# Kernel tuning notes

Measured on AMD Instinct MI355X. Metric: run time of the kernel, lower is better.

## Reference

```python
import jax, jax.numpy as jnp
import numpy as np

H, D = 16, 64  # num_heads, head_dim (hidden = H*D = 1024)
EPS = 1e-6

def elu_plus_one(x):
    return jax.nn.elu(x) + 1.0

def setup_inputs() -> dict:
    key = jax.random.key(0)
    ks = jax.random.split(key, 12)
    hid = H * D
    s = 0.02
    return {
        "hidden_states": jax.random.normal(ks[0], (1, 2048, hid), jnp.float32),
        "w_q": jax.random.normal(ks[1], (hid, hid), jnp.float32) * s,
        "w_k": jax.random.normal(ks[2], (hid, hid), jnp.float32) * s,
        "w_v": jax.random.normal(ks[3], (hid, hid), jnp.float32) * s,
        "w_o": jax.random.normal(ks[4], (hid, hid), jnp.float32) * s,
        "memory_gate": jnp.zeros((H,), jnp.float32),
        "eg_w1": jax.random.normal(ks[5], (hid, hid // 4), jnp.float32) * s,
        "eg_b1": jnp.zeros((hid // 4,), jnp.float32),
        "eg_w2": jax.random.normal(ks[6], (hid // 4, 1), jnp.float32) * s,
        "eg_b2": jnp.zeros((1,), jnp.float32),
        "fine_mem": jax.random.normal(ks[7], (4, H, D, D), jnp.float32) * s,
        "fine_norm": jax.random.uniform(ks[8], (4, H, D), jnp.float32),
    }

def _retrieve(sigma_q, memory, memory_norm):
    # sigma_q: [b,h,s,d], memory: [h,d,e], memory_norm: [h,d]
    a = jnp.einsum('bhsd,hde->bhse', sigma_q, memory)
    relevance = jnp.einsum('bhsd,hd->bhs', sigma_q, memory_norm)
    out = a / jnp.clip(relevance, EPS, None)[..., None]
    return out, relevance

def reference(hidden_states, w_q, w_k, w_v, w_o, memory_gate,
              eg_w1, eg_b1, eg_w2, eg_b2, fine_mem, fine_norm):
    B, S, hid = hidden_states.shape
    def proj(w):
        return (hidden_states @ w).reshape(B, S, H, D).transpose(0, 2, 1, 3)  # [b,h,s,d]
    q, k, v = proj(w_q), proj(w_k), proj(w_v)
    sigma_q = elu_plus_one(q)

    # coarse memory = sum of fine memories
    M_coarse = fine_mem.sum(0)        # [h,d,d]
    z_coarse = fine_norm.sum(0)       # [h,d]
    output_coarse, _ = _retrieve(sigma_q, M_coarse, z_coarse)  # [b,h,s,d]

    # learned expansion gate on coarse representation
    coarse_repr = output_coarse.transpose(0, 2, 1, 3).reshape(B, S, hid)
    logit = jax.nn.relu(coarse_repr @ eg_w1 + eg_b1) @ eg_w2 + eg_b2  # [b,s,1]
    expansion_prob = jax.nn.sigmoid(logit)                            # [b,s,1]

    # fine-grained retrieval: attention-weighted mix over the 4 banks
    outs = jnp.einsum('bhsd,fhde->fbhse', sigma_q, fine_mem)   # [f,b,h,s,d]
    rels = jnp.einsum('bhsd,fhd->fbhs', sigma_q, fine_norm)    # [f,b,h,s]
    outs = outs / jnp.clip(rels, EPS, None)[..., None]
    weights = jax.nn.softmax(rels.mean(-1), axis=0)            # [f,b,h]
    output_fine = (outs * weights[:, :, :, None, None]).sum(0)  # [b,h,s,d]

    ep = expansion_prob.transpose(0, 2, 1)[..., None]          # [b,1,s,1]
    memory_output = ep * output_fine + (1.0 - ep) * output_coarse

    # causal linear attention within current segment
    sigma_k = elu_plus_one(k)
    kv = jnp.einsum('bhsd,bhse->bhsde', sigma_k, v)            # [b,h,s,d,d]
    kv_cumsum = jnp.cumsum(kv, axis=2)
    k_cumsum = jnp.cumsum(sigma_k, axis=2)
    num = jnp.einsum('bhsd,bhsde->bhse', sigma_q, kv_cumsum)
    den = jnp.clip(jnp.einsum('bhsd,bhsd->bhs', sigma_q, k_cumsum), EPS, None)[..., None]
    local_output = num / den

    gate = jax.nn.sigmoid(memory_gate).reshape(1, H, 1, 1)
    output = gate * memory_output + (1.0 - gate) * local_output
    output = output.transpose(0, 2, 1, 3).reshape(B, S, hid)
    return output @ w_o
```

## Files before the change

kernel.cpp:

```cpp
#include <hip/hip_runtime.h>
#include <cmath>

#define EPSF 1e-6f
#define LDK 72


typedef __attribute__((ext_vector_type(8))) short bf16x8;
typedef __attribute__((ext_vector_type(4))) float f32x4;
typedef __attribute__((ext_vector_type(8))) unsigned short u16x8;

__device__ __forceinline__ float wave_allsum(float v) {
#pragma unroll
  for (int off = 32; off > 0; off >>= 1) v += __shfl_xor(v, off, 64);
  return v;
}

__device__ __forceinline__ unsigned short f2bf(float f) {
  unsigned int u = __float_as_uint(f);
  unsigned int r = (u + 0x7fffu + ((u >> 16) & 1u)) >> 16;
  return (unsigned short)r;
}
__device__ __forceinline__ float bf2f(unsigned short u) {
  return __uint_as_float(((unsigned int)u) << 16);
}

__global__ __launch_bounds__(256) void k0_mcT(const float* __restrict__ FM,
    const float* __restrict__ FN, unsigned short* __restrict__ MCT,
    float* __restrict__ ZC)
{
  int h = blockIdx.x, q = blockIdx.y, tid = threadIdx.x;
  __shared__ float tile[16][65];
  for (int i = tid; i < 1024; i += 256) {
    int dpl = i >> 6, e = i & 63;
    int idx = (q * 16 + dpl) * 64 + e;
    float s = FM[(0 * 16 + h) * 4096 + idx] + FM[(1 * 16 + h) * 4096 + idx]
            + FM[(2 * 16 + h) * 4096 + idx] + FM[(3 * 16 + h) * 4096 + idx];
    tile[dpl][e] = s;
  }
  if (q == 0 && tid < 64)
    ZC[h * 64 + tid] = FN[h * 64 + tid] + FN[1024 + h * 64 + tid]
                     + FN[2048 + h * 64 + tid] + FN[3072 + h * 64 + tid];
  __syncthreads();
  for (int i = tid; i < 1024; i += 256) {
    int e = i >> 4, dpl = i & 15;
    MCT[h * 4096 + e * 64 + q * 16 + dpl] = f2bf(tile[dpl][e]);
  }
}

__global__ __launch_bounds__(256) void cast_bf16_k(const float* __restrict__ X,
    unsigned short* __restrict__ Y)
{
  int i = blockIdx.x * 256 + threadIdx.x;
  float4 v = *reinterpret_cast<const float4*>(X + i * 4);
  ushort4 o; o.x = f2bf(v.x); o.y = f2bf(v.y); o.z = f2bf(v.z); o.w = f2bf(v.w);
  *reinterpret_cast<ushort4*>(Y + i * 4) = o;
}

__global__ __launch_bounds__(256) void cast_transpose_k(const float* __restrict__ W,
    unsigned short* __restrict__ WT, int N)
{
  __shared__ float tile[64][65];
  int n0 = blockIdx.x * 64, k0 = blockIdx.y * 64;
  int tid = threadIdx.x;
  for (int i = tid; i < 4096; i += 256) {
    int r = i >> 6, c = i & 63;
    tile[r][c] = W[(k0 + r) * N + n0 + c];
  }
  __syncthreads();
  for (int i = tid; i < 1024; i += 256) {
    int r = i >> 4, c4 = (i & 15) * 4;
    ushort4 o;
    o.x = f2bf(tile[c4 + 0][r]); o.y = f2bf(tile[c4 + 1][r]);
    o.z = f2bf(tile[c4 + 2][r]); o.w = f2bf(tile[c4 + 3][r]);
    *reinterpret_cast<ushort4*>(&WT[(n0 + r) * 1024 + k0 + c4]) = o;
  }
}

__global__ __launch_bounds__(256) void cast_w4(const float* __restrict__ W0,
    const float* __restrict__ W1, const float* __restrict__ W2, const float* __restrict__ W3,
    unsigned short* __restrict__ T0, unsigned short* __restrict__ T1,
    unsigned short* __restrict__ T2, unsigned short* __restrict__ T3)
{
  int z = blockIdx.z;
  const float* W = (z == 0) ? W0 : (z == 1) ? W1 : (z == 2) ? W2 : W3;
  unsigned short* WT = (z == 0) ? T0 : (z == 1) ? T1 : (z == 2) ? T2 : T3;
  __shared__ float tile[64][65];
  int n0 = blockIdx.x * 64, k0 = blockIdx.y * 64;
  int tid = threadIdx.x;
  for (int i = tid; i < 4096; i += 256) {
    int r = i >> 6, c = i & 63;
    tile[r][c] = W[(k0 + r) * 1024 + n0 + c];
  }
  __syncthreads();
  for (int i = tid; i < 1024; i += 256) {
    int r = i >> 4, c4 = (i & 15) * 4;
    ushort4 o;
    o.x = f2bf(tile[c4 + 0][r]); o.y = f2bf(tile[c4 + 1][r]);
    o.z = f2bf(tile[c4 + 2][r]); o.w = f2bf(tile[c4 + 3][r]);
    *reinterpret_cast<ushort4*>(&WT[(n0 + r) * 1024 + k0 + c4]) = o;
  }
}

__global__ __launch_bounds__(256) void fm_cast_t(const float* __restrict__ FM,
    unsigned short* __restrict__ FMT)
{
  __shared__ float tile[64][65];
  int b = blockIdx.x, tid = threadIdx.x;
  const float* src = FM + b * 4096;
  for (int i = tid; i < 4096; i += 256) tile[i >> 6][i & 63] = src[i];
  __syncthreads();
  unsigned short* dst = FMT + b * 4096;
  for (int i = tid; i < 4096; i += 256) {
    int e = i >> 6, dp = i & 63;
    dst[e * 64 + dp] = f2bf(tile[dp][e]);
  }
}

__global__ __launch_bounds__(256) void mm_bf16(const unsigned short* __restrict__ A,
    const unsigned short* __restrict__ BT, float* __restrict__ C, int ldc, int act)
{
  __shared__ unsigned short As[128 * LDK];
  __shared__ unsigned short Bs[128 * LDK];
  int tid = threadIdx.x;
  int m0 = blockIdx.y * 128, n0 = blockIdx.x * 128;
  int wid = tid >> 6, lane = tid & 63;
  int wr = wid >> 1, wc = wid & 1;
  int lr = lane & 15, lg = lane >> 4;

  f32x4 acc[4][4];
#pragma unroll
  for (int m = 0; m < 4; ++m)
#pragma unroll
    for (int n = 0; n < 4; ++n)
#pragma unroll
      for (int r = 0; r < 4; ++r) acc[m][n][r] = 0.f;

  for (int kt = 0; kt < 16; ++kt) {
    int k0 = kt * 64;
#pragma unroll
    for (int p = 0; p < 4; ++p) {
      int c = p * 256 + tid;
      int row = c >> 3, k8 = c & 7;
      u16x8 va = *reinterpret_cast<const u16x8*>(A + (m0 + row) * 1024 + k0 + k8 * 8);
      *reinterpret_cast<u16x8*>(&As[row * LDK + k8 * 8]) = va;
      u16x8 vb = *reinterpret_cast<const u16x8*>(BT + (n0 + row) * 1024 + k0 + k8 * 8);
      *reinterpret_cast<u16x8*>(&Bs[row * LDK + k8 * 8]) = vb;
    }
    __syncthreads();
#pragma unroll
    for (int kk = 0; kk < 2; ++kk) {
      bf16x8 af[4], bfr[4];
#pragma unroll
      for (int m = 0; m < 4; ++m)
        af[m] = *reinterpret_cast<const bf16x8*>(&As[(wr * 64 + m * 16 + lr) * LDK + kk * 32 + lg * 8]);
#pragma unroll
      for (int n = 0; n < 4; ++n)
        bfr[n] = *reinterpret_cast<const bf16x8*>(&Bs[(wc * 64 + n * 16 + lr) * LDK + kk * 32 + lg * 8]);
#pragma unroll
      for (int m = 0; m < 4; ++m)
#pragma unroll
        for (int n = 0; n < 4; ++n)
          acc[m][n] = __builtin_amdgcn_mfma_f32_16x16x32_bf16(af[m], bfr[n], acc[m][n], 0, 0, 0);
    }
    __syncthreads();
  }
#pragma unroll
  for (int m = 0; m < 4; ++m)
#pragma unroll
    for (int n = 0; n < 4; ++n)
#pragma unroll
      for (int r = 0; r < 4; ++r) {
        float v = acc[m][n][r];
        if (act) v = v > 0.f ? v + 1.f : expf(v);
        C[(m0 + wr * 64 + m * 16 + lg * 4 + r) * ldc + n0 + wc * 64 + n * 16 + lr] = v;
      }
}

__global__ __launch_bounds__(256) void mm_gate_bf16(const unsigned short* __restrict__ MOB,
    const unsigned short* __restrict__ LOB, const float* __restrict__ MG,
    const unsigned short* __restrict__ BT, float* __restrict__ C)
{
  __shared__ unsigned short As[128 * LDK];
  __shared__ unsigned short Bs[128 * LDK];
  __shared__ float gs[16];
  int tid = threadIdx.x;
  int m0 = blockIdx.y * 128, n0 = blockIdx.x * 128;
  int wid = tid >> 6, lane = tid & 63;
  int wr = wid >> 1, wc = wid & 1;
  int lr = lane & 15, lg = lane >> 4;
  if (tid < 16) gs[tid] = 1.f / (1.f + expf(-MG[tid]));
  __syncthreads();

  f32x4 acc[4][4];
#pragma unroll
  for (int m = 0; m < 4; ++m)
#pragma unroll
    for (int n = 0; n < 4; ++n)
#pragma unroll
      for (int r = 0; r < 4; ++r) acc[m][n][r] = 0.f;

  for (int kt = 0; kt < 16; ++kt) {
    int k0 = kt * 64;
#pragma unroll
    for (int p = 0; p < 4; ++p) {
      int c = p * 256 + tid;
      int row = c >> 3, k8 = c & 7;
      int col = k0 + k8 * 8;
      float g = gs[col >> 6];
      u16x8 mv = *reinterpret_cast<const u16x8*>(MOB + (m0 + row) * 1024 + col);
      u16x8 lv = *reinterpret_cast<const u16x8*>(LOB + (m0 + row) * 1024 + col);
      u16x8 o;
#pragma unroll
      for (int j = 0; j < 8; ++j)
        o[j] = f2bf(g * bf2f((unsigned short)mv[j]) + (1.f - g) * bf2f((unsigned short)lv[j]));
      *reinterpret_cast<u16x8*>(&As[row * LDK + k8 * 8]) = o;
      u16x8 vb = *reinterpret_cast<const u16x8*>(BT + (n0 + row) * 1024 + k0 + k8 * 8);
      *reinterpret_cast<u16x8*>(&Bs[row * LDK + k8 * 8]) = vb;
    }
    __syncthreads();
#pragma unroll
    for (int kk = 0; kk < 2; ++kk) {
      bf16x8 af[4], bfr[4];
#pragma unroll
      for (int m = 0; m < 4; ++m)
        af[m] = *reinterpret_cast<const bf16x8*>(&As[(wr * 64 + m * 16 + lr) * LDK + kk * 32 + lg * 8]);
#pragma unroll
      for (int n = 0; n < 4; ++n)
        bfr[n] = *reinterpret_cast<const bf16x8*>(&Bs[(wc * 64 + n * 16 + lr) * LDK + kk * 32 + lg * 8]);
#pragma unroll
      for (int m = 0; m < 4; ++m)
#pragma unroll
        for (int n = 0; n < 4; ++n)
          acc[m][n] = __builtin_amdgcn_mfma_f32_16x16x32_bf16(af[m], bfr[n], acc[m][n], 0, 0, 0);
    }
    __syncthreads();
  }
#pragma unroll
  for (int m = 0; m < 4; ++m)
#pragma unroll
    for (int n = 0; n < 4; ++n)
#pragma unroll
      for (int r = 0; r < 4; ++r)
        C[(m0 + wr * 64 + m * 16 + lg * 4 + r) * 1024 + n0 + wc * 64 + n * 16 + lr] = acc[m][n][r];
}

__global__ __launch_bounds__(256) void proj_bf16(const unsigned short* __restrict__ A,
    const unsigned short* __restrict__ WqT, const unsigned short* __restrict__ WkT,
    const unsigned short* __restrict__ WvT,
    unsigned short* __restrict__ Oq, unsigned short* __restrict__ Ok,
    unsigned short* __restrict__ Ov)
{
  int z = blockIdx.z;
  const unsigned short* BT = (z == 0) ? WqT : (z == 1) ? WkT : WvT;
  unsigned short* C = (z == 0) ? Oq : (z == 1) ? Ok : Ov;

  __shared__ unsigned short As[128 * LDK];
  __shared__ unsigned short Bs[128 * LDK];
  int tid = threadIdx.x;
  int m0 = blockIdx.y * 128, n0 = blockIdx.x * 128;
  int wid = tid >> 6, lane = tid & 63;
  int wr = wid >> 1, wc = wid & 1;
  int lr = lane & 15, lg = lane >> 4;
  int act = (z < 2) ? 1 : 0;

  f32x4 acc[4][4];
#pragma unroll
  for (int m = 0; m < 4; ++m)
#pragma unroll
    for (int n = 0; n < 4; ++n)
#pragma unroll
      for (int r = 0; r < 4; ++r) acc[m][n][r] = 0.f;

  for (int kt = 0; kt < 16; ++kt) {
    int k0 = kt * 64;
#pragma unroll
    for (int p = 0; p < 4; ++p) {
      int c = p * 256 + tid;
      int row = c >> 3, k8 = c & 7;
      u16x8 va = *reinterpret_cast<const u16x8*>(A + (m0 + row) * 1024 + k0 + k8 * 8);
      *reinterpret_cast<u16x8*>(&As[row * LDK + k8 * 8]) = va;
      u16x8 vb = *reinterpret_cast<const u16x8*>(BT + (n0 + row) * 1024 + k0 + k8 * 8);
      *reinterpret_cast<u16x8*>(&Bs[row * LDK + k8 * 8]) = vb;
    }
    __syncthreads();
#pragma unroll
    for (int kk = 0; kk < 2; ++kk) {
      bf16x8 af[4], bfr[4];
#pragma unroll
      for (int m = 0; m < 4; ++m)
        af[m] = *reinterpret_cast<const bf16x8*>(&As[(wr * 64 + m * 16 + lr) * LDK + kk * 32 + lg * 8]);
#pragma unroll
      for (int n = 0; n < 4; ++n)
        bfr[n] = *reinterpret_cast<const bf16x8*>(&Bs[(wc * 64 + n * 16 + lr) * LDK + kk * 32 + lg * 8]);
#pragma unroll
      for (int m = 0; m < 4; ++m)
#pragma unroll
        for (int n = 0; n < 4; ++n)
          acc[m][n] = __builtin_amdgcn_mfma_f32_16x16x32_bf16(af[m], bfr[n], acc[m][n], 0, 0, 0);
    }
    __syncthreads();
  }
#pragma unroll
  for (int m = 0; m < 4; ++m)
#pragma unroll
    for (int n = 0; n < 4; ++n)
#pragma unroll
      for (int r = 0; r < 4; ++r) {
        float v = acc[m][n][r];
        if (act) v = v > 0.f ? v + 1.f : expf(v);
        C[(m0 + wr * 64 + m * 16 + lg * 4 + r) * 1024 + n0 + wc * 64 + n * 16 + lr] = f2bf(v);
      }
}

__global__ __launch_bounds__(256) void eg_fin(const float* __restrict__ H1,
    const float* __restrict__ B1, const float* __restrict__ W2,
    const float* __restrict__ B2, float* __restrict__ EP)
{
  int wid = threadIdx.x >> 6, lane = threadIdx.x & 63;
  int s = blockIdx.x * 4 + wid;
  float4 h = *reinterpret_cast<const float4*>(H1 + s * 256 + lane * 4);
  float4 b = *reinterpret_cast<const float4*>(B1 + lane * 4);
  float4 w = *reinterpret_cast<const float4*>(W2 + lane * 4);
  float v = fmaxf(h.x + b.x, 0.f) * w.x + fmaxf(h.y + b.y, 0.f) * w.y
          + fmaxf(h.z + b.z, 0.f) * w.z + fmaxf(h.w + b.w, 0.f) * w.w;
  v = wave_allsum(v);
  if (lane == 0) EP[s] = 1.f / (1.f + expf(-(v + B2[0])));
}

__global__ __launch_bounds__(256) void rels_kernel(const unsigned short* __restrict__ SQB,
    const float* __restrict__ ZC, const float* __restrict__ FN,
    float* __restrict__ RELC, float* __restrict__ RELS, float* __restrict__ PARTS)
{
  int h = blockIdx.x, st = blockIdx.y, tid = threadIdx.x;
  int s0 = st * 64;
  __shared__ float sqT[64][68];
  __shared__ float zf[5][64];
  __shared__ float relb[5][64];
#pragma unroll
  for (int p = 0; p < 2; ++p) {
    int cidx = p * 256 + tid;
    int r = cidx >> 3, d8 = cidx & 7;
    u16x8 v = *reinterpret_cast<const u16x8*>(SQB + (s0 + r) * 1024 + h * 64 + d8 * 8);
#pragma unroll
    for (int j = 0; j < 8; ++j) sqT[d8 * 8 + j][r] = bf2f((unsigned short)v[j]);
  }
  for (int idx = tid; idx < 320; idx += 256) {
    int w = idx >> 6, d = idx & 63;
    zf[w][d] = (w == 0) ? ZC[h * 64 + d] : FN[(w - 1) * 1024 + h * 64 + d];
  }
  __syncthreads();
  {
    int s = tid & 63, wh = tid >> 6;
    float r = 0.f;
    for (int dp = 0; dp < 64; ++dp) r += sqT[dp][s] * zf[wh][dp];
    relb[wh][s] = r;
    if (wh == 0) {
      float r4 = 0.f;
      for (int dp = 0; dp < 64; ++dp) r4 += sqT[dp][s] * zf[4][dp];
      relb[4][s] = r4;
    }
  }
  __syncthreads();
  if (tid < 64) {
    RELC[h * 2048 + s0 + tid] = relb[0][tid];
#pragma unroll
    for (int f = 0; f < 4; ++f)
      RELS[f * 32768 + h * 2048 + s0 + tid] = relb[1 + f][tid];
#pragma unroll
    for (int f = 0; f < 4; ++f) {
      float v = wave_allsum(relb[1 + f][tid]);
      if (tid == 0) PARTS[f * 512 + h * 32 + st] = v;
    }
  }
}

__global__ __launch_bounds__(256) void coarse_mfma(const unsigned short* __restrict__ SQB,
    const unsigned short* __restrict__ MCT, const float* __restrict__ RELC,
    unsigned short* __restrict__ COB)
{
  int h = blockIdx.x, st = blockIdx.y, tid = threadIdx.x;
  int w = tid >> 6, lane = tid & 63, lr = lane & 15, lg = lane >> 4;
  int s0 = st * 128;
  __shared__ unsigned short A_lds[128 * LDK];
  __shared__ unsigned short B_lds[64 * LDK];
#pragma unroll
  for (int p = 0; p < 4; ++p) {
    int c = p * 256 + tid;
    int row = c >> 3, k8 = c & 7;
    *reinterpret_cast<u16x8*>(&A_lds[row * LDK + k8 * 8]) =
        *reinterpret_cast<const u16x8*>(SQB + (s0 + row) * 1024 + h * 64 + k8 * 8);
  }
#pragma unroll
  for (int p = 0; p < 2; ++p) {
    int c = p * 256 + tid;
    int e = c >> 3, k8 = c & 7;
    *reinterpret_cast<u16x8*>(&B_lds[e * LDK + k8 * 8]) =
        *reinterpret_cast<const u16x8*>(MCT + h * 4096 + e * 64 + k8 * 8);
  }
  __syncthreads();

  f32x4 acc[2][4];
#pragma unroll
  for (int m = 0; m < 2; ++m)
#pragma unroll
    for (int n = 0; n < 4; ++n)
#pragma unroll
      for (int r = 0; r < 4; ++r) acc[m][n][r] = 0.f;

#pragma unroll
  for (int kk = 0; kk < 2; ++kk) {
    bf16x8 af[2], bfr[4];
#pragma unroll
    for (int m = 0; m < 2; ++m)
      af[m] = *reinterpret_cast<const bf16x8*>(&A_lds[(w * 32 + m * 16 + lr) * LDK + kk * 32 + lg * 8]);
#pragma unroll
    for (int n = 0; n < 4; ++n)
      bfr[n] = *reinterpret_cast<const bf16x8*>(&B_lds[(n * 16 + lr) * LDK + kk * 32 + lg * 8]);
#pragma unroll
    for (int m = 0; m < 2; ++m)
#pragma unroll
      for (int n = 0; n < 4; ++n)
        acc[m][n] = __builtin_amdgcn_mfma_f32_16x16x32_bf16(af[m], bfr[n], acc[m][n], 0, 0, 0);
  }
#pragma unroll
  for (int m = 0; m < 2; ++m)
#pragma unroll
    for (int r = 0; r < 4; ++r) {
      int s = s0 + w * 32 + m * 16 + lg * 4 + r;
      float rc = fmaxf(RELC[h * 2048 + s], EPSF);
#pragma unroll
      for (int n = 0; n < 4; ++n)
        COB[s * 1024 + h * 64 + n * 16 + lr] = f2bf(acc[m][n][r] / rc);
    }
}

__global__ __launch_bounds__(256) void fine_mfma(const unsigned short* __restrict__ SQB,
    const unsigned short* __restrict__ FMT, const float* __restrict__ RELS,
    const float* __restrict__ PARTS, const float* __restrict__ EP,
    const unsigned short* __restrict__ COB, unsigned short* __restrict__ MOB)
{
  int h = blockIdx.x, st = blockIdx.y;
  int tid = threadIdx.x;
  int w = tid >> 6, lane = tid & 63;
  int lr = lane & 15, lg = lane >> 4;
  int s0 = st * 128;

  __shared__ unsigned short A_lds[128 * LDK];
  __shared__ unsigned short B_lds[4 * 64 * LDK];
  __shared__ float rmean[4];
  if (tid < 4) {
    float s = 0.f;
    for (int t = 0; t < 32; ++t) s += PARTS[tid * 512 + h * 32 + t];
    rmean[tid] = s * (1.f / 2048.f);
  }

#pragma unroll
  for (int p = 0; p < 4; ++p) {
    int c = p * 256 + tid;
    int row = c >> 3, k8 = c & 7;
    *reinterpret_cast<u16x8*>(&A_lds[row * LDK + k8 * 8]) =
        *reinterpret_cast<const u16x8*>(SQB + (s0 + row) * 1024 + h * 64 + k8 * 8);
  }
#pragma unroll
  for (int p = 0; p < 8; ++p) {
    int c = p * 256 + tid;
    int f = c >> 9, rem = c & 511;
    int e = rem >> 3, k8 = rem & 7;
    *reinterpret_cast<u16x8*>(&B_lds[(f * 64 + e) * LDK + k8 * 8]) =
        *reinterpret_cast<const u16x8*>(FMT + (f * 16 + h) * 4096 + e * 64 + k8 * 8);
  }
  __syncthreads();

  f32x4 acc[4][2][4];
#pragma unroll
  for (int f = 0; f < 4; ++f)
#pragma unroll
    for (int m = 0; m < 2; ++m)
#pragma unroll
      for (int n = 0; n < 4; ++n)
#pragma unroll
        for (int r = 0; r < 4; ++r) acc[f][m][n][r] = 0.f;

#pragma unroll
  for (int kk = 0; kk < 2; ++kk) {
    bf16x8 af[2];
#pragma unroll
    for (int m = 0; m < 2; ++m)
      af[m] = *reinterpret_cast<const bf16x8*>(&A_lds[(w * 32 + m * 16 + lr) * LDK + kk * 32 + lg * 8]);
#pragma unroll
    for (int f = 0; f < 4; ++f) {
      bf16x8 bf4[4];
#pragma unroll
      for (int n = 0; n < 4; ++n)
        bf4[n] = *reinterpret_cast<const bf16x8*>(&B_lds[(f * 64 + n * 16 + lr) * LDK + kk * 32 + lg * 8]);
#pragma unroll
      for (int m = 0; m < 2; ++m)
#pragma unroll
        for (int n = 0; n < 4; ++n)
          acc[f][m][n] = __builtin_amdgcn_mfma_f32_16x16x32_bf16(af[m], bf4[n], acc[f][m][n], 0, 0, 0);
    }
  }

  float rm = fmaxf(fmaxf(rmean[0], rmean[1]), fmaxf(rmean[2], rmean[3]));
  float e0 = expf(rmean[0] - rm), e1 = expf(rmean[1] - rm);
  float e2 = expf(rmean[2] - rm), e3 = expf(rmean[3] - rm);
  float winv = 1.f / (e0 + e1 + e2 + e3);
  float w0 = e0 * winv, w1 = e1 * winv, w2 = e2 * winv, w3 = e3 * winv;

#pragma unroll
  for (int m = 0; m < 2; ++m)
#pragma unroll
    for (int r = 0; r < 4; ++r) {
      int s = s0 + w * 32 + m * 16 + lg * 4 + r;
      float e = EP[s];
      float i0 = w0 / fmaxf(RELS[0 * 32768 + h * 2048 + s], EPSF);
      float i1 = w1 / fmaxf(RELS[1 * 32768 + h * 2048 + s], EPSF);
      float i2 = w2 / fmaxf(RELS[2 * 32768 + h * 2048 + s], EPSF);
      float i3 = w3 / fmaxf(RELS[3 * 32768 + h * 2048 + s], EPSF);
#pragma unroll
      for (int n = 0; n < 4; ++n) {
        int dg = h * 64 + n * 16 + lr;
        float fine = acc[0][m][n][r] * i0 + acc[1][m][n][r] * i1
                   + acc[2][m][n][r] * i2 + acc[3][m][n][r] * i3;
        float cv = bf2f(COB[s * 1024 + dg]);
        MOB[s * 1024 + dg] = f2bf(e * fine + (1.f - e) * cv);
      }
    }
}

__global__ __launch_bounds__(256) void chunk_mfma(const unsigned short* __restrict__ SKB,
    const unsigned short* __restrict__ VVB, float* __restrict__ ST)
{
  int h = blockIdx.x, c = blockIdx.y, tid = threadIdx.x;
  int w = tid >> 6, lane = tid & 63, lr = lane & 15, lg = lane >> 4;
  int sb = c * 64;
  __shared__ unsigned short A_lds[64 * LDK];
  __shared__ unsigned short B_lds[80 * LDK];
#pragma unroll
  for (int p = 0; p < 2; ++p) {
    int cc = p * 256 + tid;
    int t = cc >> 3, e8 = cc & 7;
    u16x8 kv = *reinterpret_cast<const u16x8*>(SKB + (sb + t) * 1024 + h * 64 + e8 * 8);
    u16x8 vv = *reinterpret_cast<const u16x8*>(VVB + (sb + t) * 1024 + h * 64 + e8 * 8);
#pragma unroll
    for (int j = 0; j < 8; ++j) {
      A_lds[(e8 * 8 + j) * LDK + t] = (unsigned short)kv[j];
      B_lds[(e8 * 8 + j) * LDK + t] = (unsigned short)vv[j];
    }
  }
  if (tid < 64) B_lds[64 * LDK + tid] = 0x3F80;
  for (int i = tid; i < 15 * 64; i += 256) {
    int row = 65 + (i >> 6), col = i & 63;
    B_lds[row * LDK + col] = 0;
  }
  __syncthreads();

  f32x4 acc[5];
#pragma unroll
  for (int n = 0; n < 5; ++n)
#pragma unroll
    for (int r = 0; r < 4; ++r) acc[n][r] = 0.f;
#pragma unroll
  for (int kk = 0; kk < 2; ++kk) {
    bf16x8 af = *reinterpret_cast<const bf16x8*>(&A_lds[(w * 16 + lr) * LDK + kk * 32 + lg * 8]);
#pragma unroll
    for (int n = 0; n < 5; ++n) {
      bf16x8 bfr = *reinterpret_cast<const bf16x8*>(&B_lds[(n * 16 + lr) * LDK + kk * 32 + lg * 8]);
      acc[n] = __builtin_amdgcn_mfma_f32_16x16x32_bf16(af, bfr, acc[n], 0, 0, 0);
    }
  }
  float* base = ST + (h * 32 + c) * 4160;
#pragma unroll
  for (int r = 0; r < 4; ++r) {
    int d = w * 16 + lg * 4 + r;
#pragma unroll
    for (int n = 0; n < 4; ++n)
      base[d * 64 + n * 16 + lr] = acc[n][r];
    if (lr == 0) base[4096 + d] = acc[4][r];
  }
}

__global__ __launch_bounds__(256) void scan_kernel(const float* __restrict__ ST,
    unsigned short* __restrict__ STB)
{
  int gidx = blockIdx.x * 256 + threadIdx.x;
  int h = gidx / 4160, idx = gidx - h * 4160;
  if (h >= 16) return;
  float run = 0.f;
#pragma unroll 4
  for (int c = 0; c < 32; ++c) {
    float t = ST[(h * 32 + c) * 4160 + idx];
    STB[(h * 32 + c) * 4160 + idx] = f2bf(run);
    run += t;
  }
}

__global__ __launch_bounds__(256) void lattn_mfma(const unsigned short* __restrict__ SQB,
    const unsigned short* __restrict__ SKB, const unsigned short* __restrict__ VVB,
    const unsigned short* __restrict__ STB, unsigned short* __restrict__ LOB)
{
  int h = blockIdx.x, c = blockIdx.y, tid = threadIdx.x;
  int w = tid >> 6, lane = tid & 63, lr = lane & 15, lg = lane >> 4;
  int sb = c * 64;
  const unsigned short* stb = STB + (h * 32 + c) * 4160;

  __shared__ unsigned short A_lds[64 * LDK];
  __shared__ unsigned short K_lds[64 * LDK];
  __shared__ unsigned short P_lds[80 * LDK];
  __shared__ unsigned short V_lds[80 * LDK];
  __shared__ unsigned short S_lds[64 * LDK];

#pragma unroll
  for (int p = 0; p < 2; ++p) {
    int cc = p * 256 + tid;
    int row = cc >> 3, k8 = cc & 7;
    *reinterpret_cast<u16x8*>(&A_lds[row * LDK + k8 * 8]) =
        *reinterpret_cast<const u16x8*>(SQB + (sb + row) * 1024 + h * 64 + k8 * 8);
    *reinterpret_cast<u16x8*>(&K_lds[row * LDK + k8 * 8]) =
        *reinterpret_cast<const u16x8*>(SKB + (sb + row) * 1024 + h * 64 + k8 * 8);
  }
  for (int i = tid; i < 4096; i += 256) {
    int d = i >> 6, e = i & 63;
    P_lds[e * LDK + d] = stb[i];
  }
#pragma unroll
  for (int p = 0; p < 2; ++p) {
    int cc = p * 256 + tid;
    int t = cc >> 3, e8 = cc & 7;
    u16x8 v = *reinterpret_cast<const u16x8*>(VVB + (sb + t) * 1024 + h * 64 + e8 * 8);
#pragma unroll
    for (int j = 0; j < 8; ++j) V_lds[(e8 * 8 + j) * LDK + t] = (unsigned short)v[j];
  }
  if (tid < 64) {
    P_lds[64 * LDK + tid] = stb[4096 + tid];
    V_lds[64 * LDK + tid] = 0x3F80;
  }
  for (int i = tid; i < 15 * 64; i += 256) {
    int row = 65 + (i >> 6), col = i & 63;
    P_lds[row * LDK + col] = 0;
    V_lds[row * LDK + col] = 0;
  }
  __syncthreads();

  f32x4 acc_i[5];
#pragma unroll
  for (int n = 0; n < 5; ++n)
#pragma unroll
    for (int r = 0; r < 4; ++r) acc_i[n][r] = 0.f;
#pragma unroll
  for (int kk = 0; kk < 2; ++kk) {
    bf16x8 af = *reinterpret_cast<const bf16x8*>(&A_lds[(w * 16 + lr) * LDK + kk * 32 + lg * 8]);
#pragma unroll
    for (int n = 0; n < 5; ++n) {
      bf16x8 bfr = *reinterpret_cast<const bf16x8*>(&P_lds[(n * 16 + lr) * LDK + kk * 32 + lg * 8]);
      acc_i[n] = __builtin_amdgcn_mfma_f32_16x16x32_bf16(af, bfr, acc_i[n], 0, 0, 0);
    }
  }
  f32x4 acc_s[4];
#pragma unroll
  for (int n = 0; n < 4; ++n)
#pragma unroll
    for (int r = 0; r < 4; ++r) acc_s[n][r] = 0.f;
#pragma unroll
  for (int kk = 0; kk < 2; ++kk) {
    bf16x8 af = *reinterpret_cast<const bf16x8*>(&A_lds[(w * 16 + lr) * LDK + kk * 32 + lg * 8]);
#pragma unroll
    for (int n = 0; n < 4; ++n) {
      bf16x8 bfr = *reinterpret_cast<const bf16x8*>(&K_lds[(n * 16 + lr) * LDK + kk * 32 + lg * 8]);
      acc_s[n] = __builtin_amdgcn_mfma_f32_16x16x32_bf16(af, bfr, acc_s[n], 0, 0, 0);
    }
  }
#pragma unroll
  for (int n = 0; n < 4; ++n)
#pragma unroll
    for (int r = 0; r < 4; ++r) {
      int s_loc = w * 16 + lg * 4 + r, t = n * 16 + lr;
      float v = (t <= s_loc) ? acc_s[n][r] : 0.f;
      S_lds[s_loc * LDK + t] = f2bf(v);
    }
  __syncthreads();
  f32x4 acc_p[5];
#pragma unroll
  for (int n = 0; n < 5; ++n)
#pragma unroll
    for (int r = 0; r < 4; ++r) acc_p[n][r] = 0.f;
#pragma unroll
  for (int kk = 0; kk < 2; ++kk) {
    bf16x8 af = *reinterpret_cast<const bf16x8*>(&S_lds[(w * 16 + lr) * LDK + kk * 32 + lg * 8]);
#pragma unroll
    for (int n = 0; n < 5; ++n) {
      bf16x8 bfr = *reinterpret_cast<const bf16x8*>(&V_lds[(n * 16 + lr) * LDK + kk * 32 + lg * 8]);
      acc_p[n] = __builtin_amdgcn_mfma_f32_16x16x32_bf16(af, bfr, acc_p[n], 0, 0, 0);
    }
  }
#pragma unroll
  for (int r = 0; r < 4; ++r) {
    float den = acc_i[4][r] + acc_p[4][r];
    den = __shfl(den, lane & 48);
    den = fmaxf(den, EPSF);
    int s = sb + w * 16 + lg * 4 + r;
#pragma unroll
    for (int n = 0; n < 4; ++n)
      LOB[s * 1024 + h * 64 + n * 16 + lr] = f2bf((acc_i[n][r] + acc_p[n][r]) / den);
  }
}

extern "C" void kernel_launch(void* const* d_in, const int* in_sizes, int n_in,
                              void* d_out, int out_size, void* d_ws, size_t ws_size,
                              hipStream_t stream)
{
  const float* hs   = (const float*)d_in[0];
  const float* wq   = (const float*)d_in[1];
  const float* wk   = (const float*)d_in[2];
  const float* wv   = (const float*)d_in[3];
  const float* wo   = (const float*)d_in[4];
  const float* mg   = (const float*)d_in[5];
  const float* egw1 = (const float*)d_in[6];
  const float* egb1 = (const float*)d_in[7];
  const float* egw2 = (const float*)d_in[8];
  const float* egb2 = (const float*)d_in[9];
  const float* fm   = (const float*)d_in[10];
  const float* fn   = (const float*)d_in[11];
  float* out = (float*)d_out;

  float* ws     = (float*)d_ws;
  float* zc     = ws;
  float* rels   = zc + 1024;
  float* parts  = rels + 131072;
  float* ep     = parts + 2048;
  float* relc   = ep + 2048;
  float* states = relc + 32768;
  float* h1     = states + 2129920;
  unsigned short* hsb  = (unsigned short*)(h1 + 524288);
  unsigned short* sqb  = hsb + 2097152;
  unsigned short* skb  = sqb + 2097152;
  unsigned short* vvb  = skb + 2097152;
  unsigned short* cob  = vvb + 2097152;
  unsigned short* mob  = cob + 2097152;
  unsigned short* lob  = mob + 2097152;
  unsigned short* wqT  = lob + 2097152;
  unsigned short* wkT  = wqT + 1048576;
  unsigned short* wvT  = wkT + 1048576;
  unsigned short* woT  = wvT + 1048576;
  unsigned short* w1T  = woT + 1048576;
  unsigned short* fmbT = w1T + 262144;
  unsigned short* mcT  = fmbT + 262144;
  unsigned short* statesb = mcT + 65536;

  k0_mcT<<<dim3(16, 4), 256, 0, stream>>>(fm, fn, mcT, zc);
  cast_w4<<<dim3(16, 16, 4), 256, 0, stream>>>(wq, wk, wv, wo, wqT, wkT, wvT, woT);
  cast_transpose_k<<<dim3(4, 16), 256, 0, stream>>>(egw1, w1T, 256);
  fm_cast_t<<<64, 256, 0, stream>>>(fm, fmbT);
  cast_bf16_k<<<2048, 256, 0, stream>>>(hs, hsb);
  proj_bf16<<<dim3(8, 16, 3), 256, 0, stream>>>(hsb, wqT, wkT, wvT, sqb, skb, vvb);
  rels_kernel<<<dim3(16, 32), 256, 0, stream>>>(sqb, zc, fn, relc, rels, parts);
  coarse_mfma<<<dim3(16, 16), 256, 0, stream>>>(sqb, mcT, relc, cob);
  mm_bf16<<<dim3(2, 16), 256, 0, stream>>>(cob, w1T, h1, 256, 0);
  eg_fin<<<512, 256, 0, stream>>>(h1, egb1, egw2, egb2, ep);
  fine_mfma<<<dim3(16, 16), 256, 0, stream>>>(sqb, fmbT, rels, parts, ep, cob, mob);
  chunk_mfma<<<dim3(16, 32), 256, 0, stream>>>(skb, vvb, states);
  scan_kernel<<<260, 256, 0, stream>>>(states, statesb);
  lattn_mfma<<<dim3(16, 32), 256, 0, stream>>>(sqb, skb, vvb, statesb, lob);
  mm_gate_bf16<<<dim3(8, 16), 256, 0, stream>>>(mob, lob, mg, woT, out);
}
```

Before: 142.1 us.

## Fuse prep kernels and compute relevance via extra MFMA in retrieval kernels

Result: slower. 148.2 us (+4.3%).

```diff
diff --git a/kernel.cpp b/kernel.cpp
--- a/kernel.cpp
+++ b/kernel.cpp
@@ -24,95 +24,85 @@
   return __uint_as_float(((unsigned int)u) << 16);
 }
 
-__global__ __launch_bounds__(256) void k0_mcT(const float* __restrict__ FM,
-    const float* __restrict__ FN, unsigned short* __restrict__ MCT,
-    float* __restrict__ ZC)
-{
-  int h = blockIdx.x, q = blockIdx.y, tid = threadIdx.x;
-  __shared__ float tile[16][65];
-  for (int i = tid; i < 1024; i += 256) {
-    int dpl = i >> 6, e = i & 63;
-    int idx = (q * 16 + dpl) * 64 + e;
-    float s = FM[(0 * 16 + h) * 4096 + idx] + FM[(1 * 16 + h) * 4096 + idx]
-            + FM[(2 * 16 + h) * 4096 + idx] + FM[(3 * 16 + h) * 4096 + idx];
-    tile[dpl][e] = s;
-  }
-  if (q == 0 && tid < 64)
-    ZC[h * 64 + tid] = FN[h * 64 + tid] + FN[1024 + h * 64 + tid]
-                     + FN[2048 + h * 64 + tid] + FN[3072 + h * 64 + tid];
-  __syncthreads();
-  for (int i = tid; i < 1024; i += 256) {
-    int e = i >> 4, dpl = i & 15;
-    MCT[h * 4096 + e * 64 + q * 16 + dpl] = f2bf(tile[dpl][e]);
-  }
-}
-
-__global__ __launch_bounds__(256) void cast_bf16_k(const float* __restrict__ X,
-    unsigned short* __restrict__ Y)
-{
-  int i = blockIdx.x * 256 + threadIdx.x;
-  float4 v = *reinterpret_cast<const float4*>(X + i * 4);
-  ushort4 o; o.x = f2bf(v.x); o.y = f2bf(v.y); o.z = f2bf(v.z); o.w = f2bf(v.w);
-  *reinterpret_cast<ushort4*>(Y + i * 4) = o;
-}
-
-__global__ __launch_bounds__(256) void cast_transpose_k(const float* __restrict__ W,
-    unsigned short* __restrict__ WT, int N)
-{
+__global__ __launch_bounds__(256) void prep_kernel(const float* __restrict__ FM,
+    const float* __restrict__ FN, const float* __restrict__ HS,
+    const float* __restrict__ W0, const float* __restrict__ W1,
+    const float* __restrict__ W2, const float* __restrict__ W3,
+    const float* __restrict__ EGW1,
+    unsigned short* __restrict__ MCT, unsigned short* __restrict__ ZCB,
+    unsigned short* __restrict__ FNB,
+    unsigned short* __restrict__ T0, unsigned short* __restrict__ T1,
+    unsigned short* __restrict__ T2, unsigned short* __restrict__ T3,
+    unsigned short* __restrict__ W1T, unsigned short* __restrict__ FMT,
+    unsigned short* __restrict__ HSB)
+{
+  int b = blockIdx.x, tid = threadIdx.x;
   __shared__ float tile[64][65];
-  int n0 = blockIdx.x * 64, k0 = blockIdx.y * 64;
-  int tid = threadIdx.x;
-  for (int i = tid; i < 4096; i += 256) {
-    int r = i >> 6, c = i & 63;
-    tile[r][c] = W[(k0 + r) * N + n0 + c];
-  }
-  __syncthreads();
-  for (int i = tid; i < 1024; i += 256) {
-    int r = i >> 4, c4 = (i & 15) * 4;
-    ushort4 o;
-    o.x = f2bf(tile[c4 + 0][r]); o.y = f2bf(tile[c4 + 1][r]);
-    o.z = f2bf(tile[c4 + 2][r]); o.w = f2bf(tile[c4 + 3][r]);
-    *reinterpret_cast<ushort4*>(&WT[(n0 + r) * 1024 + k0 + c4]) = o;
-  }
-}
-
-__global__ __launch_bounds__(256) void cast_w4(const float* __restrict__ W0,
-    const float* __restrict__ W1, const float* __restrict__ W2, const float* __restrict__ W3,
-    unsigned short* __restrict__ T0, unsigned short* __restrict__ T1,
-    unsigned short* __restrict__ T2, unsigned short* __restrict__ T3)
-{
-  int z = blockIdx.z;
-  const float* W = (z == 0) ? W0 : (z == 1) ? W1 : (z == 2) ? W2 : W3;
-  unsigned short* WT = (z == 0) ? T0 : (z == 1) ? T1 : (z == 2) ? T2 : T3;
-  __shared__ float tile[64][65];
-  int n0 = blockIdx.x * 64, k0 = blockIdx.y * 64;
-  int tid = threadIdx.x;
-  for (int i = tid; i < 4096; i += 256) {
-    int r = i >> 6, c = i & 63;
-    tile[r][c] = W[(k0 + r) * 1024 + n0 + c];
-  }
-  __syncthreads();
-  for (int i = tid; i < 1024; i += 256) {
-    int r = i >> 4, c4 = (i & 15) * 4;
-    ushort4 o;
-    o.x = f2bf(tile[c4 + 0][r]); o.y = f2bf(tile[c4 + 1][r]);
-    o.z = f2bf(tile[c4 + 2][r]); o.w = f2bf(tile[c4 + 3][r]);
-    *reinterpret_cast<ushort4*>(&WT[(n0 + r) * 1024 + k0 + c4]) = o;
-  }
-}
-
-__global__ __launch_bounds__(256) void fm_cast_t(const float* __restrict__ FM,
-    unsigned short* __restrict__ FMT)
-{
-  __shared__ float tile[64][65];
-  int b = blockIdx.x, tid = threadIdx.x;
-  const float* src = FM + b * 4096;
-  for (int i = tid; i < 4096; i += 256) tile[i >> 6][i & 63] = src[i];
-  __syncthreads();
-  unsigned short* dst = FMT + b * 4096;
-  for (int i = tid; i < 4096; i += 256) {
-    int e = i >> 6, dp = i & 63;
-    dst[e * 64 + dp] = f2bf(tile[dp][e]);
+  if (b < 64) {
+    int h = b >> 2, q = b & 3;
+    for (int i = tid; i < 1024; i += 256) {
+      int dpl = i >> 6, e = i & 63;
+      int idx = (q * 16 + dpl) * 64 + e;
+      tile[dpl][e] = FM[(0 * 16 + h) * 4096 + idx] + FM[(1 * 16 + h) * 4096 + idx]
+                   + FM[(2 * 16 + h) * 4096 + idx] + FM[(3 * 16 + h) * 4096 + idx];
+    }
+    if (q == 0 && tid < 64)
+      ZCB[h * 64 + tid] = f2bf(FN[h * 64 + tid] + FN[1024 + h * 64 + tid]
+                             + FN[2048 + h * 64 + tid] + FN[3072 + h * 64 + tid]);
+    __syncthreads();
+    for (int i = tid; i < 1024; i += 256) {
+      int e = i >> 4, dpl = i & 15;
+      MCT[h * 4096 + e * 64 + q * 16 + dpl] = f2bf(tile[dpl][e]);
+    }
+  } else if (b == 64) {
+    for (int i = tid; i < 4096; i += 256) FNB[i] = f2bf(FN[i]);
+  } else if (b < 1089) {
+    int r0 = b - 65, z = r0 >> 8, rem = r0 & 255;
+    const float* W = (z == 0) ? W0 : (z == 1) ? W1 : (z == 2) ? W2 : W3;
+    unsigned short* WT = (z == 0) ? T0 : (z == 1) ? T1 : (z == 2) ? T2 : T3;
+    int n0 = (rem & 15) * 64, k0 = (rem >> 4) * 64;
+    for (int i = tid; i < 4096; i += 256) {
+      int r = i >> 6, c = i & 63;
+      tile[r][c] = W[(k0 + r) * 1024 + n0 + c];
+    }
+    __syncthreads();
+    for (int i = tid; i < 1024; i += 256) {
+      int r = i >> 4, c4 = (i & 15) * 4;
+      ushort4 o;
+      o.x = f2bf(tile[c4 + 0][r]); o.y = f2bf(tile[c4 + 1][r]);
+      o.z = f2bf(tile[c4 + 2][r]); o.w = f2bf(tile[c4 + 3][r]);
+      *reinterpret_cast<ushort4*>(&WT[(n0 + r) * 1024 + k0 + c4]) = o;
+    }
+  } else if (b < 1153) {
+    int rem = b - 1089;
+    int n0 = (rem & 3) * 64, k0 = (rem >> 2) * 64;
+    for (int i = tid; i < 4096; i += 256) {
+      int r = i >> 6, c = i & 63;
+      tile[r][c] = EGW1[(k0 + r) * 256 + n0 + c];
+    }
+    __syncthreads();
+    for (int i = tid; i < 1024; i += 256) {
+      int r = i >> 4, c4 = (i & 15) * 4;
+      ushort4 o;
+      o.x = f2bf(tile[c4 + 0][r]); o.y = f2bf(tile[c4 + 1][r]);
+      o.z = f2bf(tile[c4 + 2][r]); o.w = f2bf(tile[c4 + 3][r]);
+      *reinterpret_cast<ushort4*>(&W1T[(n0 + r) * 1024 + k0 + c4]) = o;
+    }
+  } else if (b < 1217) {
+    int mat = b - 1153;
+    const float* src = FM + mat * 4096;
+    for (int i = tid; i < 4096; i += 256) tile[i >> 6][i & 63] = src[i];
+    __syncthreads();
+    unsigned short* dst = FMT + mat * 4096;
+    for (int i = tid; i < 4096; i += 256) {
+      int e = i >> 6, dp = i & 63;
+      dst[e * 64 + dp] = f2bf(tile[dp][e]);
+    }
+  } else {
+    int i = (b - 1217) * 256 + tid;
+    float4 v = *reinterpret_cast<const float4*>(HS + i * 4);
+    ushort4 o; o.x = f2bf(v.x); o.y = f2bf(v.y); o.z = f2bf(v.z); o.w = f2bf(v.w);
+    *reinterpret_cast<ushort4*>(HSB + i * 4) = o;
   }
 }
 
@@ -312,6 +302,23 @@
       }
 }
 
+__global__ __launch_bounds__(256) void qsum_kernel(const unsigned short* __restrict__ SQB,
+    float* __restrict__ QP)
+{
+  int h = blockIdx.x, sb = blockIdx.y, tid = threadIdx.x;
+  int d = tid & 63, g = tid >> 6;
+  float s = 0.f;
+  for (int i = 0; i < 64; ++i) {
+    int row = sb * 256 + g * 64 + i;
+    s += bf2f(SQB[row * 1024 + h * 64 + d]);
+  }
+  __shared__ float part[4][64];
+  part[g][d] = s;
+  __syncthreads();
+  if (g == 0)
+    QP[h * 512 + sb * 64 + d] = part[0][d] + part[1][d] + part[2][d] + part[3][d];
+}
+
 __global__ __launch_bounds__(256) void eg_fin(const float* __restrict__ H1,
     const float* __restrict__ B1, const float* __restrict__ W2,
     const float* __restrict__ B2, float* __restrict__ EP)
@@ -327,55 +334,8 @@
   if (lane == 0) EP[s] = 1.f / (1.f + expf(-(v + B2[0])));
 }
 
-__global__ __launch_bounds__(256) void rels_kernel(const unsigned short* __restrict__ SQB,
-    const float* __restrict__ ZC, const float* __restrict__ FN,
-    float* __restrict__ RELC, float* __restrict__ RELS, float* __restrict__ PARTS)
-{
-  int h = blockIdx.x, st = blockIdx.y, tid = threadIdx.x;
-  int s0 = st * 64;
-  __shared__ float sqT[64][68];
-  __shared__ float zf[5][64];
-  __shared__ float relb[5][64];
-#pragma unroll
-  for (int p = 0; p < 2; ++p) {
-    int cidx = p * 256 + tid;
-    int r = cidx >> 3, d8 = cidx & 7;
-    u16x8 v = *reinterpret_cast<const u16x8*>(SQB + (s0 + r) * 1024 + h * 64 + d8 * 8);
-#pragma unroll
-    for (int j = 0; j < 8; ++j) sqT[d8 * 8 + j][r] = bf2f((unsigned short)v[j]);
-  }
-  for (int idx = tid; idx < 320; idx += 256) {
-    int w = idx >> 6, d = idx & 63;
-    zf[w][d] = (w == 0) ? ZC[h * 64 + d] : FN[(w - 1) * 1024 + h * 64 + d];
-  }
-  __syncthreads();
-  {
-    int s = tid & 63, wh = tid >> 6;
-    float r = 0.f;
-    for (int dp = 0; dp < 64; ++dp) r += sqT[dp][s] * zf[wh][dp];
-    relb[wh][s] = r;
-    if (wh == 0) {
-      float r4 = 0.f;
-      for (int dp = 0; dp < 64; ++dp) r4 += sqT[dp][s] * zf[4][dp];
-      relb[4][s] = r4;
-    }
-  }
-  __syncthreads();
-  if (tid < 64) {
-    RELC[h * 2048 + s0 + tid] = relb[0][tid];
-#pragma unroll
-    for (int f = 0; f < 4; ++f)
-      RELS[f * 32768 + h * 2048 + s0 + tid] = relb[1 + f][tid];
-#pragma unroll
-    for (int f = 0; f < 4; ++f) {
-      float v = wave_allsum(relb[1 + f][tid]);
-      if (tid == 0) PARTS[f * 512 + h * 32 + st] = v;
-    }
-  }
-}
-
 __global__ __launch_bounds__(256) void coarse_mfma(const unsigned short* __restrict__ SQB,
-    const unsigned short* __restrict__ MCT, const float* __restrict__ RELC,
+    const unsigned short* __restrict__ MCT, const unsigned short* __restrict__ ZCB,
     unsigned short* __restrict__ COB)
 {
   int h = blockIdx.x, st = blockIdx.y, tid = threadIdx.x;
@@ -383,6 +343,7 @@
   int s0 = st * 128;
   __shared__ unsigned short A_lds[128 * LDK];
   __shared__ unsigned short B_lds[64 * LDK];
+  __shared__ unsigned short E_lds[16 * LDK];
 #pragma unroll
   for (int p = 0; p < 4; ++p) {
     int c = p * 256 + tid;
@@ -397,19 +358,26 @@
     *reinterpret_cast<u16x8*>(&B_lds[e * LDK + k8 * 8]) =
         *reinterpret_cast<const u16x8*>(MCT + h * 4096 + e * 64 + k8 * 8);
   }
+  if (tid < 64) E_lds[tid] = ZCB[h * 64 + tid];
+  for (int i = tid; i < 15 * 64; i += 256)
+    E_lds[(1 + (i >> 6)) * LDK + (i & 63)] = 0;
   __syncthreads();
 
-  f32x4 acc[2][4];
-#pragma unroll
-  for (int m = 0; m < 2; ++m)
+  f32x4 acc[2][4], acc_e[2];
+#pragma unroll
+  for (int m = 0; m < 2; ++m) {
 #pragma unroll
     for (int n = 0; n < 4; ++n)
 #pragma unroll
       for (int r = 0; r < 4; ++r) acc[m][n][r] = 0.f;
+#pragma unroll
+    for (int r = 0; r < 4; ++r) acc_e[m][r] = 0.f;
+  }
 
 #pragma unroll
   for (int kk = 0; kk < 2; ++kk) {
     bf16x8 af[2], bfr[4];
+    bf16x8 be = *reinterpret_cast<const bf16x8*>(&E_lds[lr * LDK + kk * 32 + lg * 8]);
 #pragma unroll
     for (int m = 0; m < 2; ++m)
       af[m] = *reinterpret_cast<const bf16x8*>(&A_lds[(w * 32 + m * 16 + lr) * LDK + kk * 32 + lg * 8]);
@@ -417,17 +385,19 @@
     for (int n = 0; n < 4; ++n)
       bfr[n] = *reinterpret_cast<const bf16x8*>(&B_lds[(n * 16 + lr) * LDK + kk * 32 + lg * 8]);
 #pragma unroll
-    for (int m = 0; m < 2; ++m)
+    for (int m = 0; m < 2; ++m) {
 #pragma unroll
       for (int n = 0; n < 4; ++n)
         acc[m][n] = __builtin_amdgcn_mfma_f32_16x16x32_bf16(af[m], bfr[n], acc[m][n], 0, 0, 0);
+      acc_e[m] = __builtin_amdgcn_mfma_f32_16x16x32_bf16(af[m], be, acc_e[m], 0, 0, 0);
+    }
   }
 #pragma unroll
   for (int m = 0; m < 2; ++m)
 #pragma unroll
     for (int r = 0; r < 4; ++r) {
       int s = s0 + w * 32 + m * 16 + lg * 4 + r;
-      float rc = fmaxf(RELC[h * 2048 + s], EPSF);
+      float rc = fmaxf(__shfl(acc_e[m][r], lane & 48), EPSF);
 #pragma unroll
       for (int n = 0; n < 4; ++n)
         COB[s * 1024 + h * 64 + n * 16 + lr] = f2bf(acc[m][n][r] / rc);
@@ -435,8 +405,8 @@
 }
 
 __global__ __launch_bounds__(256) void fine_mfma(const unsigned short* __restrict__ SQB,
-    const unsigned short* __restrict__ FMT, const float* __restrict__ RELS,
-    const float* __restrict__ PARTS, const float* __restrict__ EP,
+    const unsigned short* __restrict__ FMT, const unsigned short* __restrict__ FNB,
+    const float* __restrict__ QP, const float* __restrict__ EP,
     const unsigned short* __restrict__ COB, unsigned short* __restrict__ MOB)
 {
   int h = blockIdx.x, st = blockIdx.y;
@@ -447,11 +417,13 @@
 
   __shared__ unsigned short A_lds[128 * LDK];
   __shared__ unsigned short B_lds[4 * 64 * LDK];
+  __shared__ unsigned short E_lds[16 * LDK];
   __shared__ float rmean[4];
   if (tid < 4) {
-    float s = 0.f;
-    for (int t = 0; t < 32; ++t) s += PARTS[tid * 512 + h * 32 + t];
-    rmean[tid] = s * (1.f / 2048.f);
+    float rf = 0.f;
+    for (int i = 0; i < 512; ++i)
+      rf += QP[h * 512 + i] * bf2f(FNB[tid * 1024 + h * 64 + (i & 63)]);
+    rmean[tid] = rf * (1.f / 2048.f);
   }
 
 #pragma unroll
@@ -469,9 +441,15 @@
     *reinterpret_cast<u16x8*>(&B_lds[(f * 64 + e) * LDK + k8 * 8]) =
         *reinterpret_cast<const u16x8*>(FMT + (f * 16 + h) * 4096 + e * 64 + k8 * 8);
   }
+  {
+    int f = tid >> 6, dp = tid & 63;
+    E_lds[f * LDK + dp] = FNB[f * 1024 + h * 64 + dp];
+  }
+  for (int i = tid; i < 12 * 64; i += 256)
+    E_lds[(4 + (i >> 6)) * LDK + (i & 63)] = 0;
   __syncthreads();
 
-  f32x4 acc[4][2][4];
+  f32x4 acc[4][2][4], acc_e[2];
 #pragma unroll
   for (int f = 0; f < 4; ++f)
 #pragma unroll
@@ -480,13 +458,21 @@
       for (int n = 0; n < 4; ++n)
 #pragma unroll
         for (int r = 0; r < 4; ++r) acc[f][m][n][r] = 0.f;
+#pragma unroll
+  for (int m = 0; m < 2; ++m)
+#pragma unroll
+    for (int r = 0; r < 4; ++r) acc_e[m][r] = 0.f;
 
 #pragma unroll
   for (int kk = 0; kk < 2; ++kk) {
     bf16x8 af[2];
+    bf16x8 be = *reinterpret_cast<const bf16x8*>(&E_lds[lr * LDK + kk * 32 + lg * 8]);
 #pragma unroll
     for (int m = 0; m < 2; ++m)
       af[m] = *reinterpret_cast<const bf16x8*>(&A_lds[(w * 32 + m * 16 + lr) * LDK + kk * 32 + lg * 8]);
+#pragma unroll
+    for (int m = 0; m < 2; ++m)
+      acc_e[m] = __builtin_amdgcn_mfma_f32_16x16x32_bf16(af[m], be, acc_e[m], 0, 0, 0);
 #pragma unroll
     for (int f = 0; f < 4; ++f) {
       bf16x8 bf4[4];
@@ -513,10 +499,14 @@
     for (int r = 0; r < 4; ++r) {
       int s = s0 + w * 32 + m * 16 + lg * 4 + r;
       float e = EP[s];
-      float i0 = w0 / fmaxf(RELS[0 * 32768 + h * 2048 + s], EPSF);
-      float i1 = w1 / fmaxf(RELS[1 * 32768 + h * 2048 + s], EPSF);
-      float i2 = w2 / fmaxf(RELS[2 * 32768 + h * 2048 + s], EPSF);
-      float i3 = w3 / fmaxf(RELS[3 * 32768 + h * 2048 + s], EPSF);
+      float rel0 = __shfl(acc_e[m][r], (lane & 48) + 0);
+      float rel1 = __shfl(acc_e[m][r], (lane & 48) + 1);
+      float rel2 = __shfl(acc_e[m][r], (lane & 48) + 2);
+      float rel3 = __shfl(acc_e[m][r], (lane & 48) + 3);
+      float i0 = w0 / fmaxf(rel0, EPSF);
+      float i1 = w1 / fmaxf(rel1, EPSF);
+      float i2 = w2 / fmaxf(rel2, EPSF);
+      float i3 = w3 / fmaxf(rel3, EPSF);
 #pragma unroll
       for (int n = 0; n < 4; ++n) {
         int dg = h * 64 + n * 16 + lr;
@@ -724,12 +714,9 @@
   float* out = (float*)d_out;
 
   float* ws     = (float*)d_ws;
-  float* zc     = ws;
-  float* rels   = zc + 1024;
-  float* parts  = rels + 131072;
-  float* ep     = parts + 2048;
-  float* relc   = ep + 2048;
-  float* states = relc + 32768;
+  float* ep     = ws;
+  float* qp     = ep + 2048;
+  float* states = qp + 8192;
   float* h1     = states + 2129920;
   unsigned short* hsb  = (unsigned short*)(h1 + 524288);
   unsigned short* sqb  = hsb + 2097152;
@@ -745,19 +732,18 @@
   unsigned short* w1T  = woT + 1048576;
   unsigned short* fmbT = w1T + 262144;
   unsigned short* mcT  = fmbT + 262144;
-  unsigned short* statesb = mcT + 65536;
-
-  k0_mcT<<<dim3(16, 4), 256, 0, stream>>>(fm, fn, mcT, zc);
-  cast_w4<<<dim3(16, 16, 4), 256, 0, stream>>>(wq, wk, wv, wo, wqT, wkT, wvT, woT);
-  cast_transpose_k<<<dim3(4, 16), 256, 0, stream>>>(egw1, w1T, 256);
-  fm_cast_t<<<64, 256, 0, stream>>>(fm, fmbT);
-  cast_bf16_k<<<2048, 256, 0, stream>>>(hs, hsb);
+  unsigned short* zcb  = mcT + 65536;
+  unsigned short* fnb  = zcb + 1024;
+  unsigned short* statesb = fnb + 4096;
+
+  prep_kernel<<<3265, 256, 0, stream>>>(fm, fn, hs, wq, wk, wv, wo, egw1,
+      mcT, zcb, fnb, wqT, wkT, wvT, woT, w1T, fmbT, hsb);
   proj_bf16<<<dim3(8, 16, 3), 256, 0, stream>>>(hsb, wqT, wkT, wvT, sqb, skb, vvb);
-  rels_kernel<<<dim3(16, 32), 256, 0, stream>>>(sqb, zc, fn, relc, rels, parts);
-  coarse_mfma<<<dim3(16, 16), 256, 0, stream>>>(sqb, mcT, relc, cob);
+  qsum_kernel<<<dim3(16, 8), 256, 0, stream>>>(sqb, qp);
+  coarse_mfma<<<dim3(16, 16), 256, 0, stream>>>(sqb, mcT, zcb, cob);
   mm_bf16<<<dim3(2, 16), 256, 0, stream>>>(cob, w1T, h1, 256, 0);
   eg_fin<<<512, 256, 0, stream>>>(h1, egb1, egw2, egb2, ep);
-  fine_mfma<<<dim3(16, 16), 256, 0, stream>>>(sqb, fmbT, rels, parts, ep, cob, mob);
+  fine_mfma<<<dim3(16, 16), 256, 0, stream>>>(sqb, fmbT, fnb, qp, ep, cob, mob);
   chunk_mfma<<<dim3(16, 32), 256, 0, stream>>>(skb, vvb, states);
   scan_kernel<<<260, 256, 0, stream>>>(states, statesb);
   lattn_mfma<<<dim3(16, 32), 256, 0, stream>>>(sqb, skb, vvb, statesb, lob);
```
